# Kernel tuning notes

Hardware: AMD Instinct MI355X
Metric: run time of the kernel (lower is better)

## Reference

```python
import jax, jax.numpy as jnp
import numpy as np

N, E, C_IN, C_OUT = 50000, 800000, 16, 8
HID, HEADS, N_DRONES = 96, 4, 5000
NEG_SLOPE = 0.2


def setup_inputs() -> dict:
    key = jax.random.key(0)
    ks = jax.random.split(key, 16)
    x = jax.random.normal(ks[0], (N, C_IN), jnp.float32)
    # deterministic drone indicator in column -2: first N_DRONES nodes are drones
    x = x.at[:, -2].set(jnp.where(jnp.arange(N) < N_DRONES, -1.0, 1.0))
    edge_index = jax.random.randint(ks[1], (2, E), 0, N, dtype=jnp.int32)

    def w(k, shape, fan_in):
        return jax.random.normal(k, shape, jnp.float32) * (1.0 / np.sqrt(fan_in))

    C0 = HID // HEADS  # 24 per-head channels, layer 0 (concat=True)
    C1 = HID           # 96 per-head channels, layer 1 (concat=False)
    params = {
        'Wl0': w(ks[2], (C_IN, HEADS * C0), C_IN), 'bl0': jnp.zeros((HEADS * C0,), jnp.float32),
        'Wr0': w(ks[3], (C_IN, HEADS * C0), C_IN), 'br0': jnp.zeros((HEADS * C0,), jnp.float32),
        'att0': w(ks[4], (HEADS, C0), C0), 'b0': jnp.zeros((HEADS * C0,), jnp.float32),
        'Wl1': w(ks[5], (HID, HEADS * C1), HID), 'bl1': jnp.zeros((HEADS * C1,), jnp.float32),
        'Wr1': w(ks[6], (HID, HEADS * C1), HID), 'br1': jnp.zeros((HEADS * C1,), jnp.float32),
        'att1': w(ks[7], (HEADS, C1), C1), 'b1': jnp.zeros((C1,), jnp.float32),
        'Wlin': w(ks[8], (HID, C_OUT), HID), 'blin': jnp.zeros((C_OUT,), jnp.float32),
    }
    return {'x': x, **params, 'edge_index': edge_index}


def gatv2_layer(x, src, dst, Wl, bl, Wr, br, att, b, heads, concat):
    n = x.shape[0]
    c = Wl.shape[1] // heads
    xl = (x @ Wl + bl).reshape(n, heads, c)  # source/message transform
    xr = (x @ Wr + br).reshape(n, heads, c)  # target transform
    # GATv2 edge scoring: a . LeakyReLU(xl_j + xr_i)
    e = jax.nn.leaky_relu(xl[src] + xr[dst], NEG_SLOPE)   # [E, H, C]
    logits = jnp.einsum('ehc,hc->eh', e, att)             # [E, H]
    # softmax over incoming edges of each target node (segment softmax)
    m = jax.ops.segment_max(logits, dst, num_segments=n)
    p = jnp.exp(logits - m[dst])
    s = jax.ops.segment_sum(p, dst, num_segments=n)
    alpha = p / s[dst]                                    # [E, H]
    out = jax.ops.segment_sum(xl[src] * alpha[..., None], dst, num_segments=n)  # [N,H,C]
    out = out.reshape(n, heads * c) if concat else out.mean(axis=1)
    return out + b


def reference(x, Wl0, bl0, Wr0, br0, att0, b0,
              Wl1, bl1, Wr1, br1, att1, b1, Wlin, blin, edge_index):
    n = x.shape[0]
    loop = jnp.arange(n, dtype=edge_index.dtype)
    src = jnp.concatenate([edge_index[0], loop])  # add self-loops (PyG default)
    dst = jnp.concatenate([edge_index[1], loop])
    h = gatv2_layer(x, src, dst, Wl0, bl0, Wr0, br0, att0, b0, HEADS, True)
    h = jax.nn.relu(h)
    h = gatv2_layer(h, src, dst, Wl1, bl1, Wr1, br1, att1, b1, HEADS, False)
    h = jax.nn.relu(h)
    y = h @ Wlin + blin                                   # [N, C_OUT]
    drone_mask = x[:, -2] < 0
    return y[drone_mask]                                  # [N_DRONES, C_OUT]
```

## Files before the change

### kernel.cpp

```cpp
#include <hip/hip_runtime.h>
#include <hip/hip_fp16.h>

#define LR_NEG 0.2f

constexpr int NN   = 50000;
constexpr int EE   = 800000;
constexpr int ET   = EE + NN;
constexpr int HH   = 4;
constexpr int C1v  = 96;
constexpr int D1v  = 384;
constexpr int COUTv= 8;
constexpr int NDRv = 5000;

constexpr int NRB_PAD = 3128;
constexpr int NFRAG_A = NRB_PAD * 3 * 4 * 16;
constexpr int NBK = (NN + 63) / 64;
constexpr int NBKP = 800;
constexpr int BCHUNK = 8192;
constexpr int NCH = (ET + BCHUNK - 1) / BCHUNK;
constexpr int NWT1 = ((NN + 31) / 32) * 6;
constexpr int NWT2 = ((NDRv + 31) / 32) * 6;
constexpr int NWT_TOT = NWT1 + NWT2;

typedef __attribute__((ext_vector_type(8))) short bf16x8;
typedef __attribute__((ext_vector_type(4))) float f32x4;

__device__ __forceinline__ float lrelu2(float v) { return fmaxf(v, LR_NEG * v); }

__global__ __launch_bounds__(256) void k_bhist(const int* __restrict__ ei,
                                               int* __restrict__ bcnt) {
  __shared__ int hist[NBKP];
  const int t = threadIdx.x;
  const int e0 = blockIdx.x * BCHUNK;
  for (int b = t; b < NBK; b += 256) hist[b] = 0;
  __syncthreads();
  #pragma unroll
  for (int i = 0; i < BCHUNK / 256; ++i) {
    int e = e0 + i * 256 + t;
    if (e < ET) {
      int d = (e < EE) ? ei[EE + e] : (e - EE);
      atomicAdd(&hist[d >> 6], 1);
    }
  }
  __syncthreads();
  for (int b = t; b < NBK; b += 256) {
    int c = hist[b];
    if (c) atomicAdd(&bcnt[b * 16], c);
  }
}

__global__ __launch_bounds__(1024) void k_bscan(const int* __restrict__ bcnt,
                                                int* __restrict__ boff,
                                                int* __restrict__ bcur) {
  __shared__ int ws[16];
  const int t = threadIdx.x, lane = t & 63, w = t >> 6;
  int v = (t < NBK) ? bcnt[t * 16] : 0;
  int sc = v;
  #pragma unroll
  for (int off = 1; off < 64; off <<= 1) {
    int u = __shfl_up(sc, off);
    if (lane >= off) sc += u;
  }
  if (lane == 63) ws[w] = sc;
  __syncthreads();
  if (w == 0) {
    int ws2 = (lane < 16) ? ws[lane] : 0;
    #pragma unroll
    for (int off = 1; off < 16; off <<= 1) {
      int u = __shfl_up(ws2, off);
      if (lane >= off) ws2 += u;
    }
    if (lane < 16) ws[lane] = ws2;
  }
  __syncthreads();
  int prev = (w > 0) ? ws[w - 1] : 0;
  int incl = prev + sc;
  if (t < NBK) {
    boff[t + 1] = incl;
    bcur[t * 16] = incl - v;
  }
  if (t == 0) boff[0] = 0;
}

__global__ __launch_bounds__(256) void k_bin2(
    const int* __restrict__ ei, int* __restrict__ bcur,
    unsigned* __restrict__ pairs) {
  __shared__ unsigned pbuf[BCHUNK];
  __shared__ int hist[NBKP];
  __shared__ int base[NBKP];
  const int t = threadIdx.x;
  const int e0 = blockIdx.x * BCHUNK;
  for (int b = t; b < NBK; b += 256) hist[b] = 0;
  __syncthreads();
  #pragma unroll
  for (int i = 0; i < BCHUNK / 256; ++i) {
    int e = e0 + i * 256 + t;
    unsigned enc = 0xFFFFFFFFu;
    if (e < ET) {
      int s, d;
      if (e < EE) { s = ei[e]; d = ei[EE + e]; } else { s = e - EE; d = s; }
      int bk = d >> 6;
      enc = (unsigned)s | ((unsigned)(d & 63) << 16) | ((unsigned)bk << 22);
      atomicAdd(&hist[bk], 1);
    }
    pbuf[i * 256 + t] = enc;
  }
  __syncthreads();
  for (int b = t; b < NBK; b += 256) {
    int c = hist[b];
    base[b] = c ? atomicAdd(&bcur[b * 16], c) : 0;
    hist[b] = 0;
  }
  __syncthreads();
  #pragma unroll
  for (int i = 0; i < BCHUNK / 256; ++i) {
    unsigned enc = pbuf[i * 256 + t];
    if (enc != 0xFFFFFFFFu) {
      int bk = enc >> 22;
      int pos = base[bk] + atomicAdd(&hist[bk], 1);
      pairs[pos] = enc & 0x3FFFFFu;
    }
  }
}

__global__ __launch_bounds__(256) void k_binscat(
    const unsigned* __restrict__ pairs, const int* __restrict__ boff,
    int* __restrict__ rowptr, unsigned short* __restrict__ csrc) {
  __shared__ int cnt[64];
  __shared__ int cur[64];
  const int b = blockIdx.x, t = threadIdx.x;
  const int n0 = b * 64;
  if (t < 64) cnt[t] = 0;
  __syncthreads();
  const int base = boff[b];
  const int end  = boff[b + 1];
  for (int p = base + t; p < end; p += 256)
    atomicAdd(&cnt[pairs[p] >> 16], 1);
  __syncthreads();
  if (t < 64) {
    int c = cnt[t];
    int sc = c;
    #pragma unroll
    for (int off = 1; off < 64; off <<= 1) {
      int u = __shfl_up(sc, off);
      if (t >= off) sc += u;
    }
    int node = n0 + t;
    if (node < NN) rowptr[node + 1] = base + sc;
    cur[t] = base + sc - c;
    if (b == 0 && t == 0) rowptr[0] = 0;
  }
  __syncthreads();
  for (int p = base + t; p < end; p += 256) {
    unsigned pr = pairs[p];
    int pos = atomicAdd(&cur[pr >> 16], 1);
    csrc[pos] = (unsigned short)(pr & 0xFFFFu);
  }
}

__global__ __launch_bounds__(256) void k_gemm16_dual(
    const float* __restrict__ A, const float* __restrict__ Wl,
    const float* __restrict__ bl, const float* __restrict__ Wr,
    const float* __restrict__ br, __half* __restrict__ xl16,
    float* __restrict__ xr, int Nrows) {
  constexpr int K = 16;
  __shared__ float Ast[K][68];
  __shared__ float Bs[K][64];
  const int tid = threadIdx.x;
  const int tx = tid & 15, ty = tid >> 4;
  const int row0 = blockIdx.x * 64, col0 = blockIdx.y * 64;
  {
    int r = tid >> 2, c = tid & 3;
    int gr = row0 + r;
    float4 v = make_float4(0.f, 0.f, 0.f, 0.f);
    if (gr < Nrows) v = *(const float4*)(A + (size_t)gr * K + c * 4);
    Ast[c * 4 + 0][r] = v.x;
    Ast[c * 4 + 1][r] = v.y;
    Ast[c * 4 + 2][r] = v.z;
    Ast[c * 4 + 3][r] = v.w;
  }
  {
    int k = tid >> 4, c = tid & 15;
    int gc = col0 + c * 4;
    const float* Wp = (gc < 96) ? (Wl + (size_t)k * 96 + gc)
                                : (Wr + (size_t)k * 96 + (gc - 96));
    *(float4*)&Bs[k][c * 4] = *(const float4*)Wp;
  }
  __syncthreads();
  float acc[4][4] = {};
  #pragma unroll
  for (int k = 0; k < K; ++k) {
    float4 a = *(const float4*)&Ast[k][ty * 4];
    float4 b = *(const float4*)&Bs[k][tx * 4];
    acc[0][0] += a.x * b.x; acc[0][1] += a.x * b.y; acc[0][2] += a.x * b.z; acc[0][3] += a.x * b.w;
    acc[1][0] += a.y * b.x; acc[1][1] += a.y * b.y; acc[1][2] += a.y * b.z; acc[1][3] += a.y * b.w;
    acc[2][0] += a.z * b.x; acc[2][1] += a.z * b.y; acc[2][2] += a.z * b.z; acc[2][3] += a.z * b.w;
    acc[3][0] += a.w * b.x; acc[3][1] += a.w * b.y; acc[3][2] += a.w * b.z; acc[3][3] += a.w * b.w;
  }
  int gc = col0 + tx * 4;
  const float* bp = (gc < 96) ? (bl + gc) : (br + (gc - 96));
  float4 bv = *(const float4*)bp;
  #pragma unroll
  for (int i2 = 0; i2 < 4; ++i2) {
    int gr = row0 + ty * 4 + i2;
    if (gr < Nrows) {
      float4 o;
      o.x = acc[i2][0] + bv.x; o.y = acc[i2][1] + bv.y;
      o.z = acc[i2][2] + bv.z; o.w = acc[i2][3] + bv.w;
      if (gc < 96) {
        union { __half2 h[2]; uint2 u; } cv;
        cv.h[0] = __floats2half2_rn(o.x, o.y);
        cv.h[1] = __floats2half2_rn(o.z, o.w);
        *(uint2*)(xl16 + (size_t)gr * 96 + gc) = cv.u;
      } else {
        *(float4*)(xr + (size_t)gr * 96 + (gc - 96)) = o;
      }
    }
  }
}

__device__ __forceinline__ void rne_split(float w, short& hi, short& lo) {
  unsigned u  = __float_as_uint(w);
  unsigned rb = u + 0x7FFFu + ((u >> 16) & 1u);
  unsigned hm = rb & 0xFFFF0000u;
  float rest = w - __uint_as_float(hm);
  unsigned u2  = __float_as_uint(rest);
  unsigned rb2 = u2 + 0x7FFFu + ((u2 >> 16) & 1u);
  hi = (short)(rb >> 16);
  lo = (short)(rb2 >> 16);
}

__global__ void k_prepw2(const float* __restrict__ Wl1, const float* __restrict__ Wr1,
                         short* __restrict__ h1p, short* __restrict__ l1p,
                         short* __restrict__ h2p, short* __restrict__ l2p,
                         int* __restrict__ bcnt) {
  int t = blockIdx.x * 256 + threadIdx.x;
  if (t < NBK * 16) bcnt[t] = 0;
  if (t >= 2 * 96 * 384) return;
  bool second = t >= 96 * 384;
  int tt = second ? t - 96 * 384 : t;
  int k = tt / 384, c = tt - k * 384;
  short hi, lo;
  rne_split((second ? Wr1 : Wl1)[tt], hi, lo);
  int cg = c >> 4, r = c & 15;
  int ks = k >> 5, kk = k & 31, kg = kk >> 3, e = kk & 7;
  size_t idx = ((((size_t)cg * 3 + ks) * 4 + kg) * 16 + r) * 8 + e;
  (second ? h2p : h1p)[idx] = hi;
  (second ? l2p : l1p)[idx] = lo;
}

__global__ void k_prepa(const float* __restrict__ A, short* __restrict__ Ah,
                        short* __restrict__ Al, int Nrows) {
  int t = blockIdx.x * 256 + threadIdx.x;
  if (t >= NFRAG_A) return;
  int r  = t & 15;
  int kg = (t >> 4) & 3;
  int q  = t >> 6;
  int rb = q / 3;
  int ks = q - rb * 3;
  int row = rb * 16 + r;
  short h[8], l[8];
  if (row < Nrows) {
    const float* p = A + (size_t)row * 96 + ks * 32 + kg * 8;
    float4 a0 = *(const float4*)p;
    float4 a1 = *(const float4*)(p + 4);
    float v[8] = {a0.x, a0.y, a0.z, a0.w, a1.x, a1.y, a1.z, a1.w};
    #pragma unroll
    for (int i = 0; i < 8; ++i) rne_split(v[i], h[i], l[i]);
  } else {
    #pragma unroll
    for (int i = 0; i < 8; ++i) { h[i] = 0; l[i] = 0; }
  }
  bf16x8 hv, lv;
  #pragma unroll
  for (int i = 0; i < 8; ++i) { hv[i] = h[i]; lv[i] = l[i]; }
  ((bf16x8*)Ah)[t] = hv;
  ((bf16x8*)Al)[t] = lv;
}

__global__ __launch_bounds__(256) void k_gemm96_mfma(
    const bf16x8* __restrict__ Ah, const bf16x8* __restrict__ Al,
    const bf16x8* __restrict__ Bh1, const bf16x8* __restrict__ Bl1,
    const bf16x8* __restrict__ Bh2, const bf16x8* __restrict__ Bl2,
    const float* __restrict__ bias1, const float* __restrict__ bias2,
    __half* __restrict__ out1, float* __restrict__ out2) {
  const int nwg = gridDim.x;
  const int orig = blockIdx.x;
  const int q = nwg >> 3, rm = nwg & 7;
  const int xcd = orig & 7, loc = orig >> 3;
  const int wg = (xcd < rm ? xcd * (q + 1) : rm * (q + 1) + (xcd - rm) * q) + loc;
  int wtile = wg * 4 + (threadIdx.x >> 6);
  if (wtile >= NWT_TOT) return;
  const bool second = wtile >= NWT1;
  if (second) wtile -= NWT1;
  const bf16x8* __restrict__ Bh = second ? Bh2 : Bh1;
  const bf16x8* __restrict__ Bl = second ? Bl2 : Bl1;
  const float*  __restrict__ bias = second ? bias2 : bias1;
  const int Nrows = second ? NDRv : NN;

  const int rt = wtile / 6, ct = wtile - rt * 6;
  const int row0 = rt * 32, col0 = ct * 64;
  const int rb0 = rt * 2;
  const int lane = threadIdx.x & 63;
  const int r = lane & 15, kg = lane >> 4;

  f32x4 acc[2][4];
  #pragma unroll
  for (int i = 0; i < 2; ++i)
    #pragma unroll
    for (int j = 0; j < 4; ++j)
      acc[i][j] = (f32x4){0.f, 0.f, 0.f, 0.f};

  #pragma unroll
  for (int ks = 0; ks < 3; ++ks) {
    bf16x8 bh[4], bl[4];
    #pragma unroll
    for (int c2 = 0; c2 < 4; ++c2) {
      int idx = (((ct * 4 + c2) * 3 + ks) * 4 + kg) * 16 + r;
      bh[c2] = Bh[idx];
      bl[c2] = Bl[idx];
    }
    bf16x8 ah[2], al[2];
    #pragma unroll
    for (int rt2 = 0; rt2 < 2; ++rt2) {
      int idx = (((rb0 + rt2) * 3 + ks) * 4 + kg) * 16 + r;
      ah[rt2] = Ah[idx];
      al[rt2] = Al[idx];
    }
    #pragma unroll
    for (int rt2 = 0; rt2 < 2; ++rt2)
      #pragma unroll
      for (int c2 = 0; c2 < 4; ++c2) {
        f32x4 c = acc[rt2][c2];
        c = __builtin_amdgcn_mfma_f32_16x16x32_bf16(bh[c2], ah[rt2], c, 0, 0, 0);
        c = __builtin_amdgcn_mfma_f32_16x16x32_bf16(bh[c2], al[rt2], c, 0, 0, 0);
        c = __builtin_amdgcn_mfma_f32_16x16x32_bf16(bl[c2], ah[rt2], c, 0, 0, 0);
        acc[rt2][c2] = c;
      }
  }

  float4 bv[4];
  #pragma unroll
  for (int c2 = 0; c2 < 4; ++c2)
    bv[c2] = *(const float4*)(bias + col0 + 16 * c2 + 4 * kg);
  #pragma unroll
  for (int rt2 = 0; rt2 < 2; ++rt2) {
    int node = row0 + 16 * rt2 + r;
    if (node < Nrows) {
      if (!second) {
        __half* op = out1 + (size_t)node * 384;
        #pragma unroll
        for (int c2 = 0; c2 < 4; ++c2) {
          int wc = col0 + 16 * c2 + 4 * kg;
          f32x4 a = acc[rt2][c2];
          union { __half2 h[2]; uint2 u; } cv;
          cv.h[0] = __floats2half2_rn(a[0] + bv[c2].x, a[1] + bv[c2].y);
          cv.h[1] = __floats2half2_rn(a[2] + bv[c2].z, a[3] + bv[c2].w);
          *(uint2*)(op + wc) = cv.u;
        }
      } else {
        float* op = out2 + (size_t)node * 384;
        #pragma unroll
        for (int c2 = 0; c2 < 4; ++c2) {
          int wc = col0 + 16 * c2 + 4 * kg;
          f32x4 a = acc[rt2][c2];
          float4 o;
          o.x = a[0] + bv[c2].x; o.y = a[1] + bv[c2].y;
          o.z = a[2] + bv[c2].z; o.w = a[3] + bv[c2].w;
          *(float4*)(op + wc) = o;
        }
      }
    }
  }
}

__global__ __launch_bounds__(256) void k_fused0(
    const __half* __restrict__ xl16, const float* __restrict__ xr,
    const float* __restrict__ att,
    const int* __restrict__ rowptr, const unsigned short* __restrict__ csrc,
    const float* __restrict__ bias, float* __restrict__ out) {
  const int wid  = threadIdx.x >> 6;
  const int lane = threadIdx.x & 63;
  const int node = blockIdx.x * 4 + wid;
  const int g  = lane >> 4;
  const int gl = lane & 15;
  const int cb = 6 * gl;
  const int beg = rowptr[node], end = rowptr[node + 1];

  float2 attv[3], xrv[3];
  {
    const float* ap = att + cb;
    attv[0] = *(const float2*)(ap);
    attv[1] = *(const float2*)(ap + 2);
    attv[2] = *(const float2*)(ap + 4);
    const float* p = xr + (size_t)node * 96 + cb;
    xrv[0].x = __builtin_nontemporal_load(p);
    xrv[0].y = __builtin_nontemporal_load(p + 1);
    xrv[1].x = __builtin_nontemporal_load(p + 2);
    xrv[1].y = __builtin_nontemporal_load(p + 3);
    xrv[2].x = __builtin_nontemporal_load(p + 4);
    xrv[2].y = __builtin_nontemporal_load(p + 5);
  }

  float m = -1e30f, s = 0.f;
  float2 acc[3] = {make_float2(0.f,0.f), make_float2(0.f,0.f), make_float2(0.f,0.f)};

  int e = beg + g;
  __half2 nxt[3];
  int src_f = 0;
  if (e < end) {
    int s0 = csrc[e];
    const __half2* row = (const __half2*)(xl16 + (size_t)s0 * 96) + 3 * gl;
    nxt[0] = row[0];
    nxt[1] = row[1];
    nxt[2] = row[2];
  }
  if (e + 4 < end) src_f = csrc[e + 4];

  for (; e < end; e += 4) {
    float2 cur0 = __half22float2(nxt[0]);
    float2 cur1 = __half22float2(nxt[1]);
    float2 cur2 = __half22float2(nxt[2]);
    if (e + 4 < end) {
      const __half2* row = (const __half2*)(xl16 + (size_t)src_f * 96) + 3 * gl;
      nxt[0] = row[0];
      nxt[1] = row[1];
      nxt[2] = row[2];
      if (e + 8 < end) src_f = csrc[e + 8];
    }
    float p = attv[0].x * lrelu2(cur0.x + xrv[0].x)
            + attv[0].y * lrelu2(cur0.y + xrv[0].y)
            + attv[1].x * lrelu2(cur1.x + xrv[1].x)
            + attv[1].y * lrelu2(cur1.y + xrv[1].y)
            + attv[2].x * lrelu2(cur2.x + xrv[2].x)
            + attv[2].y * lrelu2(cur2.y + xrv[2].y);
    p += __shfl_xor(p, 1);
    p += __shfl_xor(p, 2);
    if (p > m + 8.f) {
      float sc = __expf(m - p);
      s *= sc;
      acc[0].x *= sc; acc[0].y *= sc;
      acc[1].x *= sc; acc[1].y *= sc;
      acc[2].x *= sc; acc[2].y *= sc;
      m = p;
    }
    float w = __expf(p - m);
    s += w;
    acc[0].x += w * cur0.x; acc[0].y += w * cur0.y;
    acc[1].x += w * cur1.x; acc[1].y += w * cur1.y;
    acc[2].x += w * cur2.x; acc[2].y += w * cur2.y;
  }

  #pragma unroll
  for (int st = 16; st <= 32; st <<= 1) {
    float m2 = __shfl_xor(m, st);
    float s2 = __shfl_xor(s, st);
    float a0x = __shfl_xor(acc[0].x, st), a0y = __shfl_xor(acc[0].y, st);
    float a1x = __shfl_xor(acc[1].x, st), a1y = __shfl_xor(acc[1].y, st);
    float a2x = __shfl_xor(acc[2].x, st), a2y = __shfl_xor(acc[2].y, st);
    float nm = fmaxf(m, m2);
    float c1 = __expf(m - nm), c2 = __expf(m2 - nm);
    s = s * c1 + s2 * c2;
    acc[0].x = acc[0].x * c1 + a0x * c2; acc[0].y = acc[0].y * c1 + a0y * c2;
    acc[1].x = acc[1].x * c1 + a1x * c2; acc[1].y = acc[1].y * c1 + a1y * c2;
    acc[2].x = acc[2].x * c1 + a2x * c2; acc[2].y = acc[2].y * c1 + a2y * c2;
    m = nm;
  }

  if (g == 0) {
    float inv = 1.f / s;
    const float* bp = bias + cb;
    float* op = out + (size_t)node * 96 + cb;
    #pragma unroll
    for (int k = 0; k < 3; ++k) {
      float ox = acc[k].x * inv + bp[2 * k];
      float oy = acc[k].y * inv + bp[2 * k + 1];
      ox = ox > 0.f ? ox : 0.f;
      oy = oy > 0.f ? oy : 0.f;
      *(float2*)(op + 2 * k) = make_float2(ox, oy);
    }
  }
}

template<int C, int PF>
__global__ __launch_bounds__(256) void k_fused(
    const __half* __restrict__ xl16, const float* __restrict__ xr,
    const float* __restrict__ att,
    const int* __restrict__ rowptr, const unsigned short* __restrict__ csrc,
    const float* __restrict__ bias, const float* __restrict__ Wlin,
    const float* __restrict__ blin, float* __restrict__ y) {
  constexpr int D   = HH * C;
  constexpr int NV2 = C / 2;
  constexpr int R2  = (NV2 + 15) / 16;
  const int wid  = threadIdx.x >> 6;
  const int lane = threadIdx.x & 63;
  const int node = blockIdx.x * 4 + wid;
  const int h  = lane >> 4;
  const int li = lane & 15;
  const int beg = rowptr[node], end = rowptr[node + 1];
  const int coff = h * C + 2 * li;

  float2 attv[R2], xrv[R2];
  #pragma unroll
  for (int k = 0; k < R2; ++k) {
    int c = h * C + 2 * (li + 16 * k);
    attv[k] = *(const float2*)(att + c);
    const float* p = xr + (size_t)node * D + c;
    xrv[k].x = __builtin_nontemporal_load(p);
    xrv[k].y = __builtin_nontemporal_load(p + 1);
  }

  float m = -1e30f, s = 0.f;
  float2 acc[R2];
  #pragma unroll
  for (int k = 0; k < R2; ++k) acc[k] = make_float2(0.f, 0.f);

  auto loadrow = [&](__half2 (&dst)[R2], int src) {
    const __half2* row = (const __half2*)(xl16 + (size_t)src * D) + (coff >> 1);
    #pragma unroll
    for (int k = 0; k < R2; ++k)
      dst[k] = row[16 * k];
  };

  auto update = [&](float part, const float2 (&xlv)[R2]) {
    if (part > m + 8.f) {
      float sc = __expf(m - part);
      s *= sc;
      #pragma unroll
      for (int k = 0; k < R2; ++k) { acc[k].x *= sc; acc[k].y *= sc; }
      m = part;
    }
    float w = __expf(part - m);
    s += w;
    #pragma unroll
    for (int k = 0; k < R2; ++k) {
      acc[k].x += w * xlv[k].x;
      acc[k].y += w * xlv[k].y;
    }
  };

  auto localdot = [&](const float2 (&xlv)[R2]) -> float {
    float p = 0.f;
    #pragma unroll
    for (int k = 0; k < R2; ++k) {
      float vx = xlv[k].x + xrv[k].x;
      float vy = xlv[k].y + xrv[k].y;
      p += attv[k].x * lrelu2(vx);
      p += attv[k].y * lrelu2(vy);
    }
    return p;
  };

  for (int cb = beg; cb < end; cb += 64) {
    const int ce = min(cb + 64, end);
    const int cn = ce - cb;
    int my_src = (cb + lane < ce) ? (int)csrc[cb + lane] : 0;

    __half2 ring[PF][R2];
    #pragma unroll
    for (int u = 0; u < PF; ++u)
      if (u < cn) loadrow(ring[u], __shfl(my_src, u));

    int j = 0;
    while (j + PF <= cn) {
      float2 xlv[PF][R2];
      #pragma unroll
      for (int u = 0; u < PF; ++u)
        #pragma unroll
        for (int k = 0; k < R2; ++k) xlv[u][k] = __half22float2(ring[u][k]);
      #pragma unroll
      for (int u = 0; u < PF; ++u) {
        int jn = j + u + PF;
        if (jn < cn) loadrow(ring[u], __shfl(my_src, jn));
      }
      float part[PF];
      #pragma unroll
      for (int u = 0; u < PF; ++u) part[u] = localdot(xlv[u]);
      #pragma unroll
      for (int st = 1; st < 16; st <<= 1) {
        #pragma unroll
        for (int u = 0; u < PF; ++u) part[u] += __shfl_xor(part[u], st);
      }
      #pragma unroll
      for (int u = 0; u < PF; ++u) update(part[u], xlv[u]);
      j += PF;
    }
    #pragma unroll
    for (int u = 0; u < PF; ++u) {
      if (j + u < cn) {
        float2 xlv[R2];
        #pragma unroll
        for (int k = 0; k < R2; ++k) xlv[k] = __half22float2(ring[u][k]);
        float p = localdot(xlv);
        p += __shfl_xor(p, 1);
        p += __shfl_xor(p, 2);
        p += __shfl_xor(p, 4);
        p += __shfl_xor(p, 8);
        update(p, xlv);
      }
    }
  }

  float inv = 1.f / s;
  float hrow[2 * R2];
  #pragma unroll
  for (int k = 0; k < R2; ++k) {
    float vx = acc[k].x * inv;
    float vy = acc[k].y * inv;
    vx += __shfl_xor(vx, 16); vx += __shfl_xor(vx, 32);
    vy += __shfl_xor(vy, 16); vy += __shfl_xor(vy, 32);
    int c = 2 * (li + 16 * k);
    float ox = 0.25f * vx + bias[c];
    float oy = 0.25f * vy + bias[c + 1];
    hrow[2 * k]     = ox > 0.f ? ox : 0.f;
    hrow[2 * k + 1] = oy > 0.f ? oy : 0.f;
  }
  float pj[8] = {0.f, 0.f, 0.f, 0.f, 0.f, 0.f, 0.f, 0.f};
  if (h == 0) {
    #pragma unroll
    for (int k = 0; k < R2; ++k) {
      int c = 2 * (li + 16 * k);
      #pragma unroll
      for (int t = 0; t < 2; ++t) {
        float hv = hrow[2 * k + t];
        float4 w0 = *(const float4*)(Wlin + (size_t)(c + t) * 8);
        float4 w1 = *(const float4*)(Wlin + (size_t)(c + t) * 8 + 4);
        pj[0] += hv * w0.x; pj[1] += hv * w0.y; pj[2] += hv * w0.z; pj[3] += hv * w0.w;
        pj[4] += hv * w1.x; pj[5] += hv * w1.y; pj[6] += hv * w1.z; pj[7] += hv * w1.w;
      }
    }
  }
  #pragma unroll
  for (int st = 1; st < 16; st <<= 1) {
    #pragma unroll
    for (int j = 0; j < 8; ++j) pj[j] += __shfl_xor(pj[j], st);
  }
  if (lane == 0) {
    float4 b0 = *(const float4*)(blin);
    float4 b1 = *(const float4*)(blin + 4);
    float4 o0 = make_float4(pj[0] + b0.x, pj[1] + b0.y, pj[2] + b0.z, pj[3] + b0.w);
    float4 o1 = make_float4(pj[4] + b1.x, pj[5] + b1.y, pj[6] + b1.z, pj[7] + b1.w);
    *(float4*)(y + (size_t)node * 8)     = o0;
    *(float4*)(y + (size_t)node * 8 + 4) = o1;
  }
}

extern "C" void kernel_launch(void* const* d_in, const int* in_sizes, int n_in,
                              void* d_out, int out_size, void* d_ws, size_t ws_size,
                              hipStream_t stream) {
  const float* x    = (const float*)d_in[0];
  const float* Wl0  = (const float*)d_in[1];
  const float* bl0  = (const float*)d_in[2];
  const float* Wr0  = (const float*)d_in[3];
  const float* br0  = (const float*)d_in[4];
  const float* att0 = (const float*)d_in[5];
  const float* b0   = (const float*)d_in[6];
  const float* Wl1  = (const float*)d_in[7];
  const float* bl1  = (const float*)d_in[8];
  const float* Wr1  = (const float*)d_in[9];
  const float* br1  = (const float*)d_in[10];
  const float* att1 = (const float*)d_in[11];
  const float* b1   = (const float*)d_in[12];
  const float* Wlin = (const float*)d_in[13];
  const float* blin = (const float*)d_in[14];
  const int*   ei   = (const int*)d_in[15];
  float* y = (float*)d_out;

  char* wsb = (char*)d_ws;
  size_t off = 0;
  auto alloc = [&](size_t bytes) -> void* {
    void* p = wsb + off;
    off += (bytes + 255) & ~(size_t)255;
    return p;
  };
  __half* xl016 = (__half*)alloc((size_t)NN * 96 * 2);
  float*  xr0   = (float*)alloc((size_t)NN * 96 * 4);
  float*  h0    = (float*)alloc((size_t)NN * 96 * 4);
  __half* xl116 = (__half*)alloc((size_t)NN * D1v * 2);
  float*  xr1   = (float*)alloc((size_t)NDRv * D1v * 4);
  unsigned short* csrc = (unsigned short*)alloc((size_t)ET * 2);
  unsigned* pairs = (unsigned*)alloc((size_t)ET * 4);
  int*   rowptr = (int*)alloc((size_t)(NN + 1) * 4);
  int*   bcnt   = (int*)alloc((size_t)NBK * 16 * 4);
  int*   bcur   = (int*)alloc((size_t)NBK * 16 * 4);
  int*   boff   = (int*)alloc((size_t)(NBK + 1) * 4);
  short* wl1h   = (short*)alloc((size_t)96 * 384 * 2);
  short* wl1l   = (short*)alloc((size_t)96 * 384 * 2);
  short* wr1h   = (short*)alloc((size_t)96 * 384 * 2);
  short* wr1l   = (short*)alloc((size_t)96 * 384 * 2);
  short* a1h    = (short*)alloc((size_t)NFRAG_A * 8 * 2);
  short* a1l    = (short*)alloc((size_t)NFRAG_A * 8 * 2);

  k_prepw2<<<(2 * 96 * 384 + 255) / 256, 256, 0, stream>>>(
      Wl1, Wr1, wl1h, wl1l, wr1h, wr1l, bcnt);

  k_bhist<<<NCH, 256, 0, stream>>>(ei, bcnt);
  k_bscan<<<1, 1024, 0, stream>>>(bcnt, boff, bcur);
  k_bin2<<<NCH, 256, 0, stream>>>(ei, bcur, pairs);
  k_binscat<<<NBK, 256, 0, stream>>>(pairs, boff, rowptr, csrc);

  dim3 g0((NN + 63) / 64, 3);
  k_gemm16_dual<<<g0, 256, 0, stream>>>(x, Wl0, bl0, Wr0, br0, xl016, xr0, NN);
  k_fused0<<<NN / 4, 256, 0, stream>>>(xl016, xr0, att0, rowptr, csrc, b0, h0);

  k_prepa<<<(NFRAG_A + 255) / 256, 256, 0, stream>>>(h0, a1h, a1l, NN);

  k_gemm96_mfma<<<NWT_TOT / 4, 256, 0, stream>>>(
      (const bf16x8*)a1h, (const bf16x8*)a1l,
      (const bf16x8*)wl1h, (const bf16x8*)wl1l,
      (const bf16x8*)wr1h, (const bf16x8*)wr1l,
      bl1, br1, xl116, xr1);

  k_fused<C1v, 4><<<NDRv / 4, 256, 0, stream>>>(xl116, xr1, att1, rowptr, csrc,
                                                b1, Wlin, blin, y);
}
```

Measured before the change: 151.2 us.

## Fuse bf16 hi/lo split into layer-0 aggregation and store layer-1 xr as fp16

Layer-0 aggregation now writes its ReLU output straight into the bf16 hi/lo MFMA fragment layout through shared memory, so the separate k_prepa pass and the fp32 h0 buffer go away. The padded tail fragments are zeroed in the weight-prep kernel instead. The layer-1 target transform xr1 is now stored and read as fp16 rather than fp32, which halves that traffic at some cost in precision. The gather loop in k_fused0 also prefetches two edges ahead instead of one.

```diff
diff --git a/kernel.cpp b/kernel.cpp
--- a/kernel.cpp
+++ b/kernel.cpp
@@ -14,6 +14,8 @@
 
 constexpr int NRB_PAD = 3128;
 constexpr int NFRAG_A = NRB_PAD * 3 * 4 * 16;
+constexpr int TAIL0   = 600000 * 8;
+constexpr int TAILN   = (NFRAG_A - 600000) * 8;
 constexpr int NBK = (NN + 63) / 64;
 constexpr int NBKP = 800;
 constexpr int BCHUNK = 8192;
@@ -26,6 +28,17 @@
 typedef __attribute__((ext_vector_type(4))) float f32x4;
 
 __device__ __forceinline__ float lrelu2(float v) { return fmaxf(v, LR_NEG * v); }
+
+__device__ __forceinline__ void rne_split(float w, short& hi, short& lo) {
+  unsigned u  = __float_as_uint(w);
+  unsigned rb = u + 0x7FFFu + ((u >> 16) & 1u);
+  unsigned hm = rb & 0xFFFF0000u;
+  float rest = w - __uint_as_float(hm);
+  unsigned u2  = __float_as_uint(rest);
+  unsigned rb2 = u2 + 0x7FFFu + ((u2 >> 16) & 1u);
+  hi = (short)(rb >> 16);
+  lo = (short)(rb2 >> 16);
+}
 
 __global__ __launch_bounds__(256) void k_bhist(const int* __restrict__ ei,
                                                int* __restrict__ bcnt) {
@@ -219,23 +232,17 @@
   }
 }
 
-__device__ __forceinline__ void rne_split(float w, short& hi, short& lo) {
-  unsigned u  = __float_as_uint(w);
-  unsigned rb = u + 0x7FFFu + ((u >> 16) & 1u);
-  unsigned hm = rb & 0xFFFF0000u;
-  float rest = w - __uint_as_float(hm);
-  unsigned u2  = __float_as_uint(rest);
-  unsigned rb2 = u2 + 0x7FFFu + ((u2 >> 16) & 1u);
-  hi = (short)(rb >> 16);
-  lo = (short)(rb2 >> 16);
-}
-
 __global__ void k_prepw2(const float* __restrict__ Wl1, const float* __restrict__ Wr1,
                          short* __restrict__ h1p, short* __restrict__ l1p,
                          short* __restrict__ h2p, short* __restrict__ l2p,
-                         int* __restrict__ bcnt) {
+                         int* __restrict__ bcnt,
+                         short* __restrict__ a1h, short* __restrict__ a1l) {
   int t = blockIdx.x * 256 + threadIdx.x;
   if (t < NBK * 16) bcnt[t] = 0;
+  if (t < TAILN) {
+    a1h[TAIL0 + t] = 0;
+    a1l[TAIL0 + t] = 0;
+  }
   if (t >= 2 * 96 * 384) return;
   bool second = t >= 96 * 384;
   int tt = second ? t - 96 * 384 : t;
@@ -249,41 +256,12 @@
   (second ? l2p : l1p)[idx] = lo;
 }
 
-__global__ void k_prepa(const float* __restrict__ A, short* __restrict__ Ah,
-                        short* __restrict__ Al, int Nrows) {
-  int t = blockIdx.x * 256 + threadIdx.x;
-  if (t >= NFRAG_A) return;
-  int r  = t & 15;
-  int kg = (t >> 4) & 3;
-  int q  = t >> 6;
-  int rb = q / 3;
-  int ks = q - rb * 3;
-  int row = rb * 16 + r;
-  short h[8], l[8];
-  if (row < Nrows) {
-    const float* p = A + (size_t)row * 96 + ks * 32 + kg * 8;
-    float4 a0 = *(const float4*)p;
-    float4 a1 = *(const float4*)(p + 4);
-    float v[8] = {a0.x, a0.y, a0.z, a0.w, a1.x, a1.y, a1.z, a1.w};
-    #pragma unroll
-    for (int i = 0; i < 8; ++i) rne_split(v[i], h[i], l[i]);
-  } else {
-    #pragma unroll
-    for (int i = 0; i < 8; ++i) { h[i] = 0; l[i] = 0; }
-  }
-  bf16x8 hv, lv;
-  #pragma unroll
-  for (int i = 0; i < 8; ++i) { hv[i] = h[i]; lv[i] = l[i]; }
-  ((bf16x8*)Ah)[t] = hv;
-  ((bf16x8*)Al)[t] = lv;
-}
-
 __global__ __launch_bounds__(256) void k_gemm96_mfma(
     const bf16x8* __restrict__ Ah, const bf16x8* __restrict__ Al,
     const bf16x8* __restrict__ Bh1, const bf16x8* __restrict__ Bl1,
     const bf16x8* __restrict__ Bh2, const bf16x8* __restrict__ Bl2,
     const float* __restrict__ bias1, const float* __restrict__ bias2,
-    __half* __restrict__ out1, float* __restrict__ out2) {
+    __half* __restrict__ out1, __half* __restrict__ out2) {
   const int nwg = gridDim.x;
   const int orig = blockIdx.x;
   const int q = nwg >> 3, rm = nwg & 7;
@@ -296,6 +274,7 @@
   const bf16x8* __restrict__ Bh = second ? Bh2 : Bh1;
   const bf16x8* __restrict__ Bl = second ? Bl2 : Bl1;
   const float*  __restrict__ bias = second ? bias2 : bias1;
+  __half* __restrict__ out = second ? out2 : out1;
   const int Nrows = second ? NDRv : NN;
 
   const int rt = wtile / 6, ct = wtile - rt * 6;
@@ -347,28 +326,15 @@
   for (int rt2 = 0; rt2 < 2; ++rt2) {
     int node = row0 + 16 * rt2 + r;
     if (node < Nrows) {
-      if (!second) {
-        __half* op = out1 + (size_t)node * 384;
-        #pragma unroll
-        for (int c2 = 0; c2 < 4; ++c2) {
-          int wc = col0 + 16 * c2 + 4 * kg;
-          f32x4 a = acc[rt2][c2];
-          union { __half2 h[2]; uint2 u; } cv;
-          cv.h[0] = __floats2half2_rn(a[0] + bv[c2].x, a[1] + bv[c2].y);
-          cv.h[1] = __floats2half2_rn(a[2] + bv[c2].z, a[3] + bv[c2].w);
-          *(uint2*)(op + wc) = cv.u;
-        }
-      } else {
-        float* op = out2 + (size_t)node * 384;
-        #pragma unroll
-        for (int c2 = 0; c2 < 4; ++c2) {
-          int wc = col0 + 16 * c2 + 4 * kg;
-          f32x4 a = acc[rt2][c2];
-          float4 o;
-          o.x = a[0] + bv[c2].x; o.y = a[1] + bv[c2].y;
-          o.z = a[2] + bv[c2].z; o.w = a[3] + bv[c2].w;
-          *(float4*)(op + wc) = o;
-        }
+      __half* op = out + (size_t)node * 384;
+      #pragma unroll
+      for (int c2 = 0; c2 < 4; ++c2) {
+        int wc = col0 + 16 * c2 + 4 * kg;
+        f32x4 a = acc[rt2][c2];
+        union { __half2 h[2]; uint2 u; } cv;
+        cv.h[0] = __floats2half2_rn(a[0] + bv[c2].x, a[1] + bv[c2].y);
+        cv.h[1] = __floats2half2_rn(a[2] + bv[c2].z, a[3] + bv[c2].w);
+        *(uint2*)(op + wc) = cv.u;
       }
     }
   }
@@ -378,7 +344,9 @@
     const __half* __restrict__ xl16, const float* __restrict__ xr,
     const float* __restrict__ att,
     const int* __restrict__ rowptr, const unsigned short* __restrict__ csrc,
-    const float* __restrict__ bias, float* __restrict__ out) {
+    const float* __restrict__ bias,
+    short* __restrict__ Ah, short* __restrict__ Al) {
+  __shared__ float hbuf[4][96];
   const int wid  = threadIdx.x >> 6;
   const int lane = threadIdx.x & 63;
   const int node = blockIdx.x * 4 + wid;
@@ -406,27 +374,27 @@
   float2 acc[3] = {make_float2(0.f,0.f), make_float2(0.f,0.f), make_float2(0.f,0.f)};
 
   int e = beg + g;
-  __half2 nxt[3];
-  int src_f = 0;
+  __half2 nx0[3], nx1[3];
+  int src2 = 0;
   if (e < end) {
-    int s0 = csrc[e];
-    const __half2* row = (const __half2*)(xl16 + (size_t)s0 * 96) + 3 * gl;
-    nxt[0] = row[0];
-    nxt[1] = row[1];
-    nxt[2] = row[2];
-  }
-  if (e + 4 < end) src_f = csrc[e + 4];
+    const __half2* row = (const __half2*)(xl16 + (size_t)csrc[e] * 96) + 3 * gl;
+    nx0[0] = row[0]; nx0[1] = row[1]; nx0[2] = row[2];
+  }
+  if (e + 4 < end) {
+    const __half2* row = (const __half2*)(xl16 + (size_t)csrc[e + 4] * 96) + 3 * gl;
+    nx1[0] = row[0]; nx1[1] = row[1]; nx1[2] = row[2];
+  }
+  if (e + 8 < end) src2 = csrc[e + 8];
 
   for (; e < end; e += 4) {
-    float2 cur0 = __half22float2(nxt[0]);
-    float2 cur1 = __half22float2(nxt[1]);
-    float2 cur2 = __half22float2(nxt[2]);
-    if (e + 4 < end) {
-      const __half2* row = (const __half2*)(xl16 + (size_t)src_f * 96) + 3 * gl;
-      nxt[0] = row[0];
-      nxt[1] = row[1];
-      nxt[2] = row[2];
-      if (e + 8 < end) src_f = csrc[e + 8];
+    float2 cur0 = __half22float2(nx0[0]);
+    float2 cur1 = __half22float2(nx0[1]);
+    float2 cur2 = __half22float2(nx0[2]);
+    nx0[0] = nx1[0]; nx0[1] = nx1[1]; nx0[2] = nx1[2];
+    if (e + 8 < end) {
+      const __half2* row = (const __half2*)(xl16 + (size_t)src2 * 96) + 3 * gl;
+      nx1[0] = row[0]; nx1[1] = row[1]; nx1[2] = row[2];
+      if (e + 12 < end) src2 = csrc[e + 12];
     }
     float p = attv[0].x * lrelu2(cur0.x + xrv[0].x)
             + attv[0].y * lrelu2(cur0.y + xrv[0].y)
@@ -470,21 +438,40 @@
   if (g == 0) {
     float inv = 1.f / s;
     const float* bp = bias + cb;
-    float* op = out + (size_t)node * 96 + cb;
     #pragma unroll
     for (int k = 0; k < 3; ++k) {
       float ox = acc[k].x * inv + bp[2 * k];
       float oy = acc[k].y * inv + bp[2 * k + 1];
-      ox = ox > 0.f ? ox : 0.f;
-      oy = oy > 0.f ? oy : 0.f;
-      *(float2*)(op + 2 * k) = make_float2(ox, oy);
-    }
+      hbuf[wid][cb + 2 * k]     = ox > 0.f ? ox : 0.f;
+      hbuf[wid][cb + 2 * k + 1] = oy > 0.f ? oy : 0.f;
+    }
+  }
+  __syncthreads();
+  const int t = threadIdx.x;
+  if (t < 96) {
+    int nl    = t & 3;
+    int q     = t >> 2;
+    int plane = q & 1;
+    int kskg  = q >> 1;
+    int ks = kskg >> 2, kg = kskg & 3;
+    int ch0 = ks * 32 + kg * 8;
+    bf16x8 v;
+    #pragma unroll
+    for (int j = 0; j < 8; ++j) {
+      short hi, lo;
+      rne_split(hbuf[nl][ch0 + j], hi, lo);
+      v[j] = plane ? lo : hi;
+    }
+    int rb = (blockIdx.x * 4) >> 4;
+    int r  = ((blockIdx.x * 4) & 15) + nl;
+    int idx = ((rb * 3 + ks) * 4 + kg) * 16 + r;
+    ((bf16x8*)(plane ? Al : Ah))[idx] = v;
   }
 }
 
 template<int C, int PF>
 __global__ __launch_bounds__(256) void k_fused(
-    const __half* __restrict__ xl16, const float* __restrict__ xr,
+    const __half* __restrict__ xl16, const __half* __restrict__ xr16,
     const float* __restrict__ att,
     const int* __restrict__ rowptr, const unsigned short* __restrict__ csrc,
     const float* __restrict__ bias, const float* __restrict__ Wlin,
@@ -505,9 +492,8 @@
   for (int k = 0; k < R2; ++k) {
     int c = h * C + 2 * (li + 16 * k);
     attv[k] = *(const float2*)(att + c);
-    const float* p = xr + (size_t)node * D + c;
-    xrv[k].x = __builtin_nontemporal_load(p);
-    xrv[k].y = __builtin_nontemporal_load(p + 1);
+    const __half2* p = (const __half2*)(xr16 + (size_t)node * D + c);
+    xrv[k] = __half22float2(*p);
   }
 
   float m = -1e30f, s = 0.f;
@@ -675,9 +661,8 @@
   };
   __half* xl016 = (__half*)alloc((size_t)NN * 96 * 2);
   float*  xr0   = (float*)alloc((size_t)NN * 96 * 4);
-  float*  h0    = (float*)alloc((size_t)NN * 96 * 4);
   __half* xl116 = (__half*)alloc((size_t)NN * D1v * 2);
-  float*  xr1   = (float*)alloc((size_t)NDRv * D1v * 4);
+  __half* xr116 = (__half*)alloc((size_t)NDRv * D1v * 2);
   unsigned short* csrc = (unsigned short*)alloc((size_t)ET * 2);
   unsigned* pairs = (unsigned*)alloc((size_t)ET * 4);
   int*   rowptr = (int*)alloc((size_t)(NN + 1) * 4);
@@ -692,7 +677,7 @@
   short* a1l    = (short*)alloc((size_t)NFRAG_A * 8 * 2);
 
   k_prepw2<<<(2 * 96 * 384 + 255) / 256, 256, 0, stream>>>(
-      Wl1, Wr1, wl1h, wl1l, wr1h, wr1l, bcnt);
+      Wl1, Wr1, wl1h, wl1l, wr1h, wr1l, bcnt, a1h, a1l);
 
   k_bhist<<<NCH, 256, 0, stream>>>(ei, bcnt);
   k_bscan<<<1, 1024, 0, stream>>>(bcnt, boff, bcur);
@@ -701,16 +686,14 @@
 
   dim3 g0((NN + 63) / 64, 3);
   k_gemm16_dual<<<g0, 256, 0, stream>>>(x, Wl0, bl0, Wr0, br0, xl016, xr0, NN);
-  k_fused0<<<NN / 4, 256, 0, stream>>>(xl016, xr0, att0, rowptr, csrc, b0, h0);
-
-  k_prepa<<<(NFRAG_A + 255) / 256, 256, 0, stream>>>(h0, a1h, a1l, NN);
+  k_fused0<<<NN / 4, 256, 0, stream>>>(xl016, xr0, att0, rowptr, csrc, b0, a1h, a1l);
 
   k_gemm96_mfma<<<NWT_TOT / 4, 256, 0, stream>>>(
       (const bf16x8*)a1h, (const bf16x8*)a1l,
       (const bf16x8*)wl1h, (const bf16x8*)wl1l,
       (const bf16x8*)wr1h, (const bf16x8*)wr1l,
-      bl1, br1, xl116, xr1);
-
-  k_fused<C1v, 4><<<NDRv / 4, 256, 0, stream>>>(xl116, xr1, att1, rowptr, csrc,
+      bl1, br1, xl116, xr116);
+
+  k_fused<C1v, 4><<<NDRv / 4, 256, 0, stream>>>(xl116, xr116, att1, rowptr, csrc,
                                                 b1, Wlin, blin, y);
 }
```

Result: faster. 148.1 us (-2.1%).
